# Performance work log

Hardware: AMD Instinct MI355X
Metric: run time of the kernel (lower is better)

Reference implementation:

```python
import jax, jax.numpy as jnp
import numpy as np

N = 50000
E = 800000
IN_CH = 512
OUT_CH = 64
ITERATIONS = 3  # adjacency power order; iterations-1 spmm steps


def setup_inputs() -> dict:
    key = jax.random.key(0)
    k1, k2, k3, k4, k5 = jax.random.split(key, 5)
    adj_indices = jax.random.randint(k1, (2, E), 0, N, dtype=jnp.int32)
    adj_values = jax.random.uniform(k2, (E,), dtype=jnp.float32)
    features = jax.random.normal(k3, (N, IN_CH), dtype=jnp.float32)
    # xavier-uniform init bounds
    bw = float(np.sqrt(6.0 / (IN_CH + OUT_CH)))
    weight = jax.random.uniform(k4, (IN_CH, OUT_CH), minval=-bw, maxval=bw, dtype=jnp.float32)
    bb = float(np.sqrt(6.0 / (1 + OUT_CH)))
    bias = jax.random.uniform(k5, (1, OUT_CH), minval=-bb, maxval=bb, dtype=jnp.float32)
    return {"adj_indices": adj_indices, "adj_values": adj_values,
            "features": features, "weight": weight, "bias": bias}


def reference(adj_indices, adj_values, features, weight, bias):
    # dense projection: [N, in] @ [in, out] -> [N, out]
    x = features @ weight
    # dropout is identity in eval mode (training=False)
    row, col = adj_indices[0], adj_indices[1]
    # (iterations - 1) sparse-dense matmuls: x <- A @ x
    for _ in range(ITERATIONS - 1):
        gathered = adj_values[:, None] * x[col]          # [E, out]
        x = jax.ops.segment_sum(gathered, row, num_segments=N)
    return x + bias
```

## Files before the change

kernel.cpp:

```cpp
#include <hip/hip_runtime.h>
#include <hip/hip_bf16.h>
#include <hip/hip_fp16.h>

#define NN 50000
#define INCH 512
#define OUTCH 64
#define NTILES 3125
#define MAXD 96
#define GB 782
#define SB 256

typedef __attribute__((ext_vector_type(8))) short short8;
typedef __attribute__((ext_vector_type(4))) float floatx4;

__device__ __forceinline__ unsigned packbf2(float a, float b) {
    __hip_bfloat162 h = __float22bfloat162_rn(make_float2(a, b));
    unsigned r;
    __builtin_memcpy(&r, &h, 4);
    return r;
}
__device__ __forceinline__ unsigned short f2bf(float f) {
    unsigned u = __float_as_uint(f);
    return (unsigned short)((u + 0x7FFFu + ((u >> 16) & 1u)) >> 16);
}
__device__ __forceinline__ float bf2f(unsigned short u) {
    return __uint_as_float(((unsigned)u) << 16);
}

#define WSTR 520
__global__ __launch_bounds__(256) void fused_gemm_scatter(
        const float* __restrict__ A, const float* __restrict__ B,
        unsigned short* __restrict__ C,
        const int* __restrict__ rows, const int* __restrict__ cols,
        const float* __restrict__ vals, int* __restrict__ deg,
        unsigned* __restrict__ ell, int E_) {
    __shared__ unsigned short Ws[64 * WSTR];
    const int t = threadIdx.x;

    if (blockIdx.x >= GB) {
        for (int e = (blockIdx.x - GB) * 256 + t; e < E_; e += SB * 256) {
            const int r = rows[e];
            const int slot = atomicAdd(&deg[r], 1);
            const unsigned short hv = __half_as_ushort(__float2half(vals[e]));
            if (slot < MAXD)
                ell[(size_t)r * MAXD + slot] = (unsigned)cols[e] | ((unsigned)hv << 16);
        }
        return;
    }

    const int lane = t & 63;
    const int wave = t >> 6;

    {
        const int k2 = (t >> 4) * 2;
        const int n4 = (t & 15) * 4;
#pragma unroll
        for (int c = 0; c < 16; ++c) {
            const int k = k2 + c * 32;
            const float4 w0 = *(const float4*)(B + (k + 0) * OUTCH + n4);
            const float4 w1 = *(const float4*)(B + (k + 1) * OUTCH + n4);
            *(unsigned*)&Ws[(n4 + 0) * WSTR + k] = packbf2(w0.x, w1.x);
            *(unsigned*)&Ws[(n4 + 1) * WSTR + k] = packbf2(w0.y, w1.y);
            *(unsigned*)&Ws[(n4 + 2) * WSTR + k] = packbf2(w0.z, w1.z);
            *(unsigned*)&Ws[(n4 + 3) * WSTR + k] = packbf2(w0.w, w1.w);
        }
    }
    __syncthreads();

    const int tile = blockIdx.x * 4 + wave;
    if (tile >= NTILES) return;
    const int rbase = tile * 16;
    const int frow = lane & 15;
    const int quad = lane >> 4;
    const float* Ap = A + (size_t)(rbase + frow) * INCH + quad * 8;

    floatx4 acc[4] = {floatx4{0,0,0,0}, floatx4{0,0,0,0}, floatx4{0,0,0,0}, floatx4{0,0,0,0}};

    float4 a0 = *(const float4*)(Ap);
    float4 a1 = *(const float4*)(Ap + 4);
    for (int c = 0; c < 16; ++c) {
        const float4 c0 = a0, c1 = a1;
        if (c < 15) {
            const float* An = Ap + (c + 1) * 32;
            a0 = *(const float4*)(An);
            a1 = *(const float4*)(An + 4);
        }
        uint4 au;
        au.x = packbf2(c0.x, c0.y);
        au.y = packbf2(c0.z, c0.w);
        au.z = packbf2(c1.x, c1.y);
        au.w = packbf2(c1.z, c1.w);
        const short8 af = *(const short8*)&au;
        const int koff = c * 32 + quad * 8;
#pragma unroll
        for (int f = 0; f < 4; ++f) {
            const short8 bfr = *(const short8*)&Ws[(f * 16 + frow) * WSTR + koff];
            acc[f] = __builtin_amdgcn_mfma_f32_16x16x32_bf16(af, bfr, acc[f], 0, 0, 0);
        }
    }

#pragma unroll
    for (int f = 0; f < 4; ++f) {
#pragma unroll
        for (int reg = 0; reg < 4; ++reg) {
            C[(size_t)(rbase + quad * 4 + reg) * OUTCH + f * 16 + frow] = f2bf(acc[f][reg]);
        }
    }
}

template <bool LAST>
__global__ __launch_bounds__(256) void spmm_ell(const int* __restrict__ deg,
                                                const unsigned* __restrict__ ell,
                                                const unsigned short* __restrict__ xin,
                                                void* __restrict__ xout_,
                                                const float* __restrict__ bias) {
    const int t = threadIdx.x;
    const int lane = t & 63;
    const int eslot = lane >> 4;
    const int c4 = (lane & 15) * 4;
    const int row = blockIdx.x * 4 + (t >> 6);
    const int d = deg[row];
    const unsigned* ebase = ell + (size_t)row * MAXD;
    float4 acc = make_float4(0.f, 0.f, 0.f, 0.f);
    for (int i = eslot; i < d; i += 4) {
        const unsigned p = ebase[i];
        const ushort4 xv = *(const ushort4*)(xin + (size_t)(p & 0xFFFFu) * OUTCH + c4);
        const float v = __half2float(__ushort_as_half((unsigned short)(p >> 16)));
        acc.x = fmaf(v, bf2f(xv.x), acc.x);
        acc.y = fmaf(v, bf2f(xv.y), acc.y);
        acc.z = fmaf(v, bf2f(xv.z), acc.z);
        acc.w = fmaf(v, bf2f(xv.w), acc.w);
    }
    acc.x += __shfl_xor(acc.x, 16, 64); acc.y += __shfl_xor(acc.y, 16, 64);
    acc.z += __shfl_xor(acc.z, 16, 64); acc.w += __shfl_xor(acc.w, 16, 64);
    acc.x += __shfl_xor(acc.x, 32, 64); acc.y += __shfl_xor(acc.y, 32, 64);
    acc.z += __shfl_xor(acc.z, 32, 64); acc.w += __shfl_xor(acc.w, 32, 64);
    if (eslot == 0) {
        if (LAST) {
            const float4 bv = *(const float4*)(bias + c4);
            acc.x += bv.x; acc.y += bv.y; acc.z += bv.z; acc.w += bv.w;
            *(float4*)((float*)xout_ + (size_t)row * OUTCH + c4) = acc;
        } else {
            ushort4 o;
            o.x = f2bf(acc.x); o.y = f2bf(acc.y); o.z = f2bf(acc.z); o.w = f2bf(acc.w);
            *(ushort4*)((unsigned short*)xout_ + (size_t)row * OUTCH + c4) = o;
        }
    }
}

extern "C" void kernel_launch(void* const* d_in, const int* in_sizes, int n_in,
                              void* d_out, int out_size, void* d_ws, size_t ws_size,
                              hipStream_t stream) {
    const int*   adj   = (const int*)d_in[0];
    const float* avals = (const float*)d_in[1];
    const float* feat  = (const float*)d_in[2];
    const float* W     = (const float*)d_in[3];
    const float* bias  = (const float*)d_in[4];
    float* out = (float*)d_out;

    const int E_ = in_sizes[1];
    const int* rows = adj;
    const int* cols = adj + E_;

    unsigned short* x0 = (unsigned short*)d_ws;
    unsigned short* x1 = x0 + (size_t)NN * OUTCH;
    unsigned* ell = (unsigned*)(x1 + (size_t)NN * OUTCH);
    int* deg = (int*)(ell + (size_t)NN * MAXD);

    hipMemsetAsync(deg, 0, NN * sizeof(int), stream);

    fused_gemm_scatter<<<GB + SB, 256, 0, stream>>>(feat, W, x0, rows, cols, avals,
                                                    deg, ell, E_);

    spmm_ell<false><<<NN / 4, 256, 0, stream>>>(deg, ell, x0, x1, nullptr);
    spmm_ell<true><<<NN / 4, 256, 0, stream>>>(deg, ell, x1, out, bias);
}
```

Before: 271.3 us.

## Pre-convert weights to bf16 once and read them from global in GEMM

A small prep kernel replaces the memset. It zeroes the degree array and writes a transposed bf16 copy of the weight matrix. The GEMM no longer stages all of W into a large shared-memory tile per block, which removes that repeated conversion, the barrier and the large LDS footprint, and is meant to raise occupancy (launch bounds now ask for 4 blocks). B fragments are instead loaded directly from global/L2 each k-step. The A loads are fully unrolled rather than software-pipelined. Outputs are transposed through a small per-wave LDS buffer so they are written with coalesced 16-byte stores.

Result: faster. 260.7 us (-3.9%).

```diff
diff --git a/kernel.cpp b/kernel.cpp
--- a/kernel.cpp
+++ b/kernel.cpp
@@ -27,14 +27,25 @@
     return __uint_as_float(((unsigned)u) << 16);
 }
 
-#define WSTR 520
-__global__ __launch_bounds__(256) void fused_gemm_scatter(
-        const float* __restrict__ A, const float* __restrict__ B,
+__global__ __launch_bounds__(256) void prep_kernel(const float* __restrict__ W,
+                                                   unsigned short* __restrict__ Wbf,
+                                                   int* __restrict__ deg) {
+    const int i = blockIdx.x * 256 + threadIdx.x;
+    if (i < NN) deg[i] = 0;
+    if (i < INCH * OUTCH) {
+        const int k = i >> 6;
+        const int n = i & 63;
+        Wbf[n * INCH + k] = f2bf(W[i]);
+    }
+}
+
+__global__ __launch_bounds__(256, 4) void fused_gemm_scatter(
+        const float* __restrict__ A, const unsigned short* __restrict__ Wbf,
         unsigned short* __restrict__ C,
         const int* __restrict__ rows, const int* __restrict__ cols,
         const float* __restrict__ vals, int* __restrict__ deg,
         unsigned* __restrict__ ell, int E_) {
-    __shared__ unsigned short Ws[64 * WSTR];
+    __shared__ unsigned short ldsT[4][16 * 64];
     const int t = threadIdx.x;
 
     if (blockIdx.x >= GB) {
@@ -50,61 +61,46 @@
 
     const int lane = t & 63;
     const int wave = t >> 6;
-
-    {
-        const int k2 = (t >> 4) * 2;
-        const int n4 = (t & 15) * 4;
-#pragma unroll
-        for (int c = 0; c < 16; ++c) {
-            const int k = k2 + c * 32;
-            const float4 w0 = *(const float4*)(B + (k + 0) * OUTCH + n4);
-            const float4 w1 = *(const float4*)(B + (k + 1) * OUTCH + n4);
-            *(unsigned*)&Ws[(n4 + 0) * WSTR + k] = packbf2(w0.x, w1.x);
-            *(unsigned*)&Ws[(n4 + 1) * WSTR + k] = packbf2(w0.y, w1.y);
-            *(unsigned*)&Ws[(n4 + 2) * WSTR + k] = packbf2(w0.z, w1.z);
-            *(unsigned*)&Ws[(n4 + 3) * WSTR + k] = packbf2(w0.w, w1.w);
-        }
-    }
-    __syncthreads();
-
     const int tile = blockIdx.x * 4 + wave;
     if (tile >= NTILES) return;
     const int rbase = tile * 16;
     const int frow = lane & 15;
     const int quad = lane >> 4;
     const float* Ap = A + (size_t)(rbase + frow) * INCH + quad * 8;
+    const unsigned short* Bp = Wbf + frow * INCH + quad * 8;
 
     floatx4 acc[4] = {floatx4{0,0,0,0}, floatx4{0,0,0,0}, floatx4{0,0,0,0}, floatx4{0,0,0,0}};
 
-    float4 a0 = *(const float4*)(Ap);
-    float4 a1 = *(const float4*)(Ap + 4);
+#pragma unroll
     for (int c = 0; c < 16; ++c) {
-        const float4 c0 = a0, c1 = a1;
-        if (c < 15) {
-            const float* An = Ap + (c + 1) * 32;
-            a0 = *(const float4*)(An);
-            a1 = *(const float4*)(An + 4);
-        }
+        const float4 a0 = *(const float4*)(Ap + c * 32);
+        const float4 a1 = *(const float4*)(Ap + c * 32 + 4);
+        short8 bfr[4];
+#pragma unroll
+        for (int f = 0; f < 4; ++f)
+            bfr[f] = *(const short8*)(Bp + (size_t)f * 16 * INCH + c * 32);
         uint4 au;
-        au.x = packbf2(c0.x, c0.y);
-        au.y = packbf2(c0.z, c0.w);
-        au.z = packbf2(c1.x, c1.y);
-        au.w = packbf2(c1.z, c1.w);
+        au.x = packbf2(a0.x, a0.y);
+        au.y = packbf2(a0.z, a0.w);
+        au.z = packbf2(a1.x, a1.y);
+        au.w = packbf2(a1.z, a1.w);
         const short8 af = *(const short8*)&au;
-        const int koff = c * 32 + quad * 8;
 #pragma unroll
-        for (int f = 0; f < 4; ++f) {
-            const short8 bfr = *(const short8*)&Ws[(f * 16 + frow) * WSTR + koff];
-            acc[f] = __builtin_amdgcn_mfma_f32_16x16x32_bf16(af, bfr, acc[f], 0, 0, 0);
-        }
+        for (int f = 0; f < 4; ++f)
+            acc[f] = __builtin_amdgcn_mfma_f32_16x16x32_bf16(af, bfr[f], acc[f], 0, 0, 0);
     }
 
+    unsigned short* myT = ldsT[wave];
 #pragma unroll
-    for (int f = 0; f < 4; ++f) {
+    for (int f = 0; f < 4; ++f)
 #pragma unroll
-        for (int reg = 0; reg < 4; ++reg) {
-            C[(size_t)(rbase + quad * 4 + reg) * OUTCH + f * 16 + frow] = f2bf(acc[f][reg]);
-        }
+        for (int reg = 0; reg < 4; ++reg)
+            myT[(quad * 4 + reg) * 64 + f * 16 + frow] = f2bf(acc[f][reg]);
+    unsigned short* Cw = C + (size_t)rbase * OUTCH;
+#pragma unroll
+    for (int it = 0; it < 2; ++it) {
+        const short8 v = *(const short8*)&myT[it * 512 + lane * 8];
+        *(short8*)(Cw + it * 512 + lane * 8) = v;
     }
 }
 
@@ -162,14 +158,15 @@
     const int* rows = adj;
     const int* cols = adj + E_;
 
-    unsigned short* x0 = (unsigned short*)d_ws;
-    unsigned short* x1 = x0 + (size_t)NN * OUTCH;
-    unsigned* ell = (unsigned*)(x1 + (size_t)NN * OUTCH);
+    unsigned short* x0  = (unsigned short*)d_ws;
+    unsigned short* x1  = x0 + (size_t)NN * OUTCH;
+    unsigned short* Wbf = x1 + (size_t)NN * OUTCH;
+    unsigned* ell = (unsigned*)(Wbf + (size_t)OUTCH * INCH);
     int* deg = (int*)(ell + (size_t)NN * MAXD);
 
-    hipMemsetAsync(deg, 0, NN * sizeof(int), stream);
+    prep_kernel<<<(NN + 255) / 256, 256, 0, stream>>>(W, Wbf, deg);
 
-    fused_gemm_scatter<<<GB + SB, 256, 0, stream>>>(feat, W, x0, rows, cols, avals,
+    fused_gemm_scatter<<<GB + SB, 256, 0, stream>>>(feat, Wbf, x0, rows, cols, avals,
                                                     deg, ell, E_);
 
     spmm_ell<false><<<NN / 4, 256, 0, stream>>>(deg, ell, x0, x1, nullptr);
```
